# Kernel optimization log

Measured on AMD Instinct MI355X. Metric: run time of the kernel, lower is better.

Reference implementation:

```python
import jax, jax.numpy as jnp
import numpy as np

MASK_FILL = -987654321.0


def rotate_every_two(x):
    # pairs (x0, x1) -> (-x1, x0), interleaved back along last dim
    x1 = x[..., 0::2]
    x2 = x[..., 1::2]
    return jnp.stack((-x2, x1), axis=-1).reshape(x.shape)


def setup_inputs() -> dict:
    key = jax.random.key(0)
    ks = jax.random.split(key, 6)
    b, n, dim = 64, 197, 768
    heads, dim_head = 12, 64
    inner = heads * dim_head
    x = jax.random.normal(ks[0], (b, n, dim), dtype=jnp.float32)
    pos_emb = jax.random.normal(ks[1], (1, n, dim_head), dtype=jnp.float32)
    w_qkv = jax.random.normal(ks[2], (dim, 3 * inner), dtype=jnp.float32) * (dim ** -0.5)
    scale = jnp.full((heads,), dim_head ** -0.5, dtype=jnp.float32)
    w_out = jax.random.normal(ks[3], (inner, dim), dtype=jnp.float32) * (inner ** -0.5)
    b_out = jnp.zeros((dim,), dtype=jnp.float32)
    return {"x": x, "pos_emb": pos_emb, "w_qkv": w_qkv, "scale": scale,
            "w_out": w_out, "b_out": b_out}


def reference(x, pos_emb, w_qkv, scale, w_out, b_out):
    b, n, dim = x.shape
    h = scale.shape[0]
    qkv = x @ w_qkv                         # [b, n, 3*inner]
    q, k, v = jnp.split(qkv, 3, axis=-1)
    dh = q.shape[-1] // h
    to_heads = lambda t: t.reshape(b, n, h, dh).transpose(0, 2, 1, 3)  # bhnd
    q, k, v = to_heads(q), to_heads(k), to_heads(v)

    # RoPE: pos_emb [1, n, (2 * dh/2)] -> sin/cos [n, dh/2] -> interleave to [n, dh]
    sc = pos_emb[0].reshape(n, 2, dh // 2)
    sin = jnp.repeat(sc[:, 0], 2, axis=-1)  # [n, dh]
    cos = jnp.repeat(sc[:, 1], 2, axis=-1)
    q = q * cos + rotate_every_two(q) * sin
    k = k * cos + rotate_every_two(k) * sin

    # per-head learnable scale
    dots = jnp.einsum('bhid,bhjd->bhij', q, k) * scale[None, :, None, None]
    # diagonal (LSA) mask
    eye = jnp.eye(n, dtype=bool)
    dots = jnp.where(eye, MASK_FILL, dots)

    attn = jax.nn.softmax(dots, axis=-1)
    out = jnp.einsum('bhij,bhjd->bhid', attn, v)
    out = out.transpose(0, 2, 1, 3).reshape(b, n, h * dh)
    return out @ w_out + b_out
```

## Files before the change

kernel.cpp:

```cpp
#include <hip/hip_runtime.h>
#include <math.h>

#define MASK_FILL_F (-987654321.0f)

typedef unsigned short u16;
typedef unsigned int   u32;

constexpr int Bb   = 64;
constexpr int Ntok = 197;
constexpr int Dim  = 768;
constexpr int Heads= 12;
constexpr int Dh   = 64;
constexpr int Nq3  = 2304;
constexpr int Rows = 12608;
constexpr int Mpad = 12672;

using f32x4  = __attribute__((ext_vector_type(4))) float;
using bf16x8 = __attribute__((ext_vector_type(8))) short;

__device__ __forceinline__ u16 f2bf(float f) {
  u32 u = __float_as_uint(f);
  u = (u + 0x7fffu + ((u >> 16) & 1u)) >> 16;
  return (u16)u;
}

__device__ __forceinline__ void stage16(const void* gp, void* lp) {
  __builtin_amdgcn_global_load_lds(
      (const __attribute__((address_space(1))) u32*)gp,
      (__attribute__((address_space(3))) u32*)lp, 16, 0, 0);
}

__device__ __forceinline__ int sigma6(int M) {
  return (M & 0x23) | (((M >> 3) & 1) << 4) | (((M >> 2) & 1) << 3) |
         (((M >> 4) & 1) << 2);
}

__global__ __launch_bounds__(256) void cvt_bf16(const float* __restrict__ in,
                                                u16* __restrict__ out, int n4) {
  const int i = blockIdx.x * 256 + threadIdx.x;
  if (i < n4) {
    const float4 v = *(const float4*)&in[(size_t)i * 4];
    ushort4 u;
    u.x = f2bf(v.x); u.y = f2bf(v.y); u.z = f2bf(v.z); u.w = f2bf(v.w);
    *(ushort4*)&out[(size_t)i * 4] = u;
  }
}

__global__ __launch_bounds__(256) void transpose_cvt(const float* __restrict__ in,
                                                     u16* __restrict__ out,
                                                     int R, int C) {
  __shared__ float t[32][33];
  const int c0 = blockIdx.x * 32, r0 = blockIdx.y * 32;
  const int tx = threadIdx.x & 31, ty = threadIdx.x >> 5;
#pragma unroll
  for (int rr = ty; rr < 32; rr += 8)
    t[rr][tx] = in[(size_t)(r0 + rr) * C + c0 + tx];
  __syncthreads();
#pragma unroll
  for (int cc = ty; cc < 32; cc += 8)
    out[(size_t)(c0 + cc) * R + r0 + tx] = f2bf(t[tx][cc]);
}

__global__ __launch_bounds__(256) void vtrans(const u16* __restrict__ qkvB,
                                              u16* __restrict__ vT) {
  __shared__ u16 t[64 * 72];
  const int jt = blockIdx.x, bh = blockIdx.y;
  const int b = bh / Heads, h = bh % Heads;
  const int j0 = jt * 64;
  const int tid = threadIdx.x;

  for (int idx = tid; idx < 512; idx += 256) {
    const int jr = idx >> 3, c8 = (idx & 7) * 8;
    const int j = j0 + jr;
    uint4 u = make_uint4(0u, 0u, 0u, 0u);
    if (j < Ntok)
      u = *(const uint4*)(qkvB + (size_t)(b * Ntok + j) * Nq3 + 2 * Dim + h * Dh + c8);
    *(uint4*)&t[jr * 72 + c8] = u;
  }
  __syncthreads();
  for (int idx = tid; idx < 512; idx += 256) {
    const int d = idx >> 3, j8 = (idx & 7) * 8;
    ushort4 lo, hi;
    lo.x = t[(j8 + 0) * 72 + d]; lo.y = t[(j8 + 1) * 72 + d];
    lo.z = t[(j8 + 2) * 72 + d]; lo.w = t[(j8 + 3) * 72 + d];
    hi.x = t[(j8 + 4) * 72 + d]; hi.y = t[(j8 + 5) * 72 + d];
    hi.z = t[(j8 + 6) * 72 + d]; hi.w = t[(j8 + 7) * 72 + d];
    u16* dst = vT + ((size_t)bh * 64 + d) * 256 + j0 + j8;
    *(ushort4*)dst       = lo;
    *(ushort4*)(dst + 4) = hi;
  }
}

constexpr int Kc  = 768;
constexpr int NKT = Kc / 64;

#define BARM() asm volatile("s_barrier" ::: "memory")
#define VMW4() asm volatile("s_waitcnt vmcnt(4)" ::: "memory")

#define STGA(chunk, kt, BUF) \
  stage16(Ag + (size_t)(m0 + (chunk) * 8 + srow) * Kc + (kt) * 64 + scol, \
          &As[BUF][(chunk) * 512])
#define STGB(chunk, kt, BUF) \
  stage16(Bg + (size_t)(n0 + (chunk) * 8 + srow) * Kc + (kt) * 64 + scol, \
          &Bs[BUF][(chunk) * 512])

#define RDA(BUF, MH) \
  _Pragma("unroll") for (int m_ = 0; m_ < 4; ++m_) \
  _Pragma("unroll") for (int k_ = 0; k_ < 2; ++k_) \
    af[m_][k_] = *(const bf16x8*)&As[BUF][(wr * 128 + (MH) * 64 + m_ * 16 + tx) * 64 \
                                          + (((k_ * 4 + qd) ^ sx) * 8)];
#define RDB(BUF, NH, BFR) \
  _Pragma("unroll") for (int n_ = 0; n_ < 2; ++n_) \
  _Pragma("unroll") for (int k_ = 0; k_ < 2; ++k_) \
    BFR[n_][k_] = *(const bf16x8*)&Bs[BUF][(wc * 64 + (NH) * 32 + n_ * 16 + tx) * 64 \
                                           + (((k_ * 4 + qd) ^ sx) * 8)];

#define MM(MH, NH, BFR) \
  __builtin_amdgcn_s_setprio(1); \
  _Pragma("unroll") for (int m_ = 0; m_ < 4; ++m_) \
  _Pragma("unroll") for (int n_ = 0; n_ < 2; ++n_) \
  _Pragma("unroll") for (int k_ = 0; k_ < 2; ++k_) \
    acc[(MH) * 4 + m_][(NH) * 2 + n_] = __builtin_amdgcn_mfma_f32_16x16x32_bf16( \
        af[m_][k_], BFR[n_][k_], acc[(MH) * 4 + m_][(NH) * 2 + n_], 0, 0, 0); \
  __builtin_amdgcn_s_setprio(0);

template<int MODE, int TN>
__global__ __launch_bounds__(512, 2) void gemm8p(
    const u16* __restrict__ Ag, const u16* __restrict__ Bg,
    void* __restrict__ Cv, int Nn, int nwg,
    const float* __restrict__ pe, const float* __restrict__ bias)
{
  __shared__ u16 As[2][256 * 64];
  __shared__ u16 Bs[2][256 * 64];

  const int tid = threadIdx.x, lane = tid & 63, w = tid >> 6;

  const int orig = blockIdx.x;
  const int q8 = nwg >> 3, r8 = nwg & 7;
  const int xcd = orig & 7, sub = orig >> 3;
  const int wgid = (xcd < r8 ? xcd * (q8 + 1) : r8 * (q8 + 1) + (xcd - r8) * q8) + sub;
  const int tm = wgid / TN, tn = wgid % TN;
  const int m0 = tm * 256, n0 = tn * 256;

  const int wr = w >> 2, wc = w & 3;
  const int tx = lane & 15, qd = lane >> 4, sx = tx & 7;

  const int srow = lane >> 3;
  const int scol = ((lane & 7) ^ srow) * 8;
  const int b0 = (w >> 1) * 8 + (w & 1) * 2;

  STGA(w, 0, 0);        STGA(16 + w, 0, 0);
  STGB(b0 + 4, 0, 0);   STGB(b0 + 5, 0, 0);
  STGA(8 + w, 0, 0);    STGA(24 + w, 0, 0);
  STGB(b0, 0, 0);       STGB(b0 + 1, 0, 0);
  STGA(w, 1, 1);        STGA(16 + w, 1, 1);
  STGB(b0 + 4, 1, 1);   STGB(b0 + 5, 1, 1);
  VMW4();
  BARM();

  f32x4  acc[8][4] = {};
  bf16x8 af[4][2], bf0[2][2], bf1[2][2];

#pragma unroll 1
  for (int i = 0; i < NKT / 2; ++i) {
    const int u = 2 * i;
    RDA(0, 0); RDB(0, 0, bf0);
    STGA(8 + w, u + 1, 1); STGA(24 + w, u + 1, 1);
    BARM(); MM(0, 0, bf0); BARM();
    RDB(0, 1, bf1);
    STGB(b0, u + 1, 1); STGB(b0 + 1, u + 1, 1);
    BARM(); MM(0, 1, bf1); BARM();
    RDA(0, 1);
    STGA(w, u + 2, 0); STGA(16 + w, u + 2, 0);
    BARM(); MM(1, 1, bf1); BARM();
    STGB(b0 + 4, u + 2, 0); STGB(b0 + 5, u + 2, 0);
    BARM(); MM(1, 0, bf0); VMW4(); BARM();
    RDA(1, 0); RDB(1, 0, bf0);
    STGA(8 + w, u + 2, 0); STGA(24 + w, u + 2, 0);
    BARM(); MM(0, 0, bf0); BARM();
    RDB(1, 1, bf1);
    STGB(b0, u + 2, 0); STGB(b0 + 1, u + 2, 0);
    BARM(); MM(0, 1, bf1); BARM();
    RDA(1, 1);
    STGA(w, u + 3, 1); STGA(16 + w, u + 3, 1);
    BARM(); MM(1, 1, bf1); BARM();
    STGB(b0 + 4, u + 3, 1); STGB(b0 + 5, u + 3, 1);
    BARM(); MM(1, 0, bf0); VMW4(); BARM();
  }

  if (MODE == 0) {
    u16* C = (u16*)Cv;
    const bool dorot = (n0 < 2 * Dim);
#pragma unroll
    for (int mi = 0; mi < 8; ++mi) {
      const int rbase = m0 + wr * 128 + mi * 16 + qd * 4;
      int iq[4];
#pragma unroll
      for (int r = 0; r < 4; ++r) iq[r] = (rbase + r) % Ntok;
#pragma unroll
      for (int ni = 0; ni < 4; ++ni) {
        const int col = n0 + wc * 64 + ni * 16 + tx;
        const int mm  = (col & 63) >> 1;
        const int odd = col & 1;
#pragma unroll
        for (int r = 0; r < 4; ++r) {
          float v = acc[mi][ni][r];
          float res = v;
          if (dorot) {
            const float other = __shfl_xor(v, 1, 64);
            const float sn = pe[iq[r] * 64 + mm];
            const float c2 = pe[iq[r] * 64 + 32 + mm];
            res = odd ? (v * c2 + other * sn) : (v * c2 - other * sn);
          }
          C[(size_t)(rbase + r) * Nn + col] = f2bf(res);
        }
      }
    }
  } else {
    float* C = (float*)Cv;
#pragma unroll
    for (int mi = 0; mi < 8; ++mi) {
      const int rbase = m0 + wr * 128 + mi * 16 + qd * 4;
#pragma unroll
      for (int ni = 0; ni < 4; ++ni) {
        const int col = n0 + wc * 64 + ni * 16 + tx;
        const float bv = bias[col];
#pragma unroll
        for (int r = 0; r < 4; ++r) {
          const int row = rbase + r;
          if (row < Rows) C[(size_t)row * Nn + col] = acc[mi][ni][r] + bv;
        }
      }
    }
  }
}

constexpr int LS = 72;

__global__ __launch_bounds__(256) void attn7(
    const u16* __restrict__ qkvB, const u16* __restrict__ vT,
    const float* __restrict__ scale, u16* __restrict__ outB)
{
  __shared__ u16 ks [64 * LS];
  __shared__ u16 vts[64 * LS];

  const int it = blockIdx.x, bh = blockIdx.y;
  const int b = bh / Heads, h = bh % Heads;
  const int i0 = it * 128;
  const float sc = scale[h];
  const int tid = threadIdx.x, lane = tid & 63, w = tid >> 6;
  const int tx = lane & 15, q = lane >> 4;
  const size_t rowbase = (size_t)b * Ntok;

  bf16x8 bq[2][2];
#pragma unroll
  for (int g = 0; g < 2; ++g)
#pragma unroll
    for (int kk = 0; kk < 2; ++kk)
      bq[g][kk] = *(const bf16x8*)(qkvB +
          (rowbase + i0 + 32 * w + 16 * g + tx) * (size_t)Nq3 + h * Dh + kk * 32 + q * 8);

  float l_part[2] = {0.f, 0.f};
  f32x4 oacc[2][4] = {};

  for (int jt = 0; jt < 4; ++jt) {
    const int j0 = jt * 64;
    __syncthreads();

    for (int idx = tid; idx < 512; idx += 256) {
      const int M = idx >> 3, c8 = (idx & 7) * 8;
      const int js = sigma6(M);
      *(uint4*)&ks[M * LS + c8] =
          *(const uint4*)(qkvB + (rowbase + j0 + js) * (size_t)Nq3 + Dim + h * Dh + c8);
    }
    for (int idx = tid; idx < 512; idx += 256) {
      const int d = idx >> 3, c8 = (idx & 7) * 8;
      *(uint4*)&vts[d * LS + c8] =
          *(const uint4*)(vT + ((size_t)bh * 64 + d) * 256 + j0 + c8);
    }
    __syncthreads();

#pragma unroll
    for (int g = 0; g < 2; ++g) {
      f32x4 sT[4] = {};
#pragma unroll
      for (int kk = 0; kk < 2; ++kk)
#pragma unroll
        for (int jb = 0; jb < 4; ++jb) {
          const bf16x8 ka = *(const bf16x8*)&ks[(jb * 16 + tx) * LS + kk * 32 + q * 8];
          sT[jb] = __builtin_amdgcn_mfma_f32_16x16x32_bf16(ka, bq[g][kk], sT[jb], 0, 0, 0);
        }

      const int ig = i0 + 32 * w + 16 * g + tx;
      union { bf16x8 v; u16 e[8]; } pk[2];
      float lp = 0.f;
#pragma unroll
      for (int jb = 0; jb < 4; ++jb)
#pragma unroll
        for (int r = 0; r < 4; ++r) {
          const int jg = j0 + 32 * (jb >> 1) + 8 * q + 4 * (jb & 1) + r;
          const float s = fminf(sT[jb][r] * sc, 80.f);
          const bool bad = (jg >= Ntok) || (jg == ig);
          const float p = bad ? 0.f : __expf(s);
          lp += p;
          pk[jb >> 1].e[(jb & 1) * 4 + r] = f2bf(p);
        }
      l_part[g] += lp;

#pragma unroll
      for (int kk = 0; kk < 2; ++kk)
#pragma unroll
        for (int nb = 0; nb < 4; ++nb) {
          const bf16x8 vb = *(const bf16x8*)&vts[(nb * 16 + tx) * LS + kk * 32 + q * 8];
          oacc[g][nb] = __builtin_amdgcn_mfma_f32_16x16x32_bf16(pk[kk].v, vb,
                                                               oacc[g][nb], 0, 0, 0);
        }
    }
  }

#pragma unroll
  for (int g = 0; g < 2; ++g) {
    float l = l_part[g];
    l += __shfl_xor(l, 16, 64);
    l += __shfl_xor(l, 32, 64);
    const float linv = 1.0f / l;
#pragma unroll
    for (int r = 0; r < 4; ++r) {
      const float lr = __shfl(linv, 4 * q + r, 64);
      const int igr = i0 + 32 * w + 16 * g + 4 * q + r;
      if (igr < Ntok) {
#pragma unroll
        for (int nb = 0; nb < 4; ++nb)
          outB[(rowbase + igr) * (size_t)Dim + h * Dh + nb * 16 + tx] =
              f2bf(oacc[g][nb][r] * lr);
      }
    }
  }
}

extern "C" void kernel_launch(void* const* d_in, const int* in_sizes, int n_in,
                              void* d_out, int out_size, void* d_ws, size_t ws_size,
                              hipStream_t stream) {
  const float* x     = (const float*)d_in[0];
  const float* pe    = (const float*)d_in[1];
  const float* w_qkv = (const float*)d_in[2];
  const float* scale = (const float*)d_in[3];
  const float* w_out = (const float*)d_in[4];
  const float* b_out = (const float*)d_in[5];
  float* out = (float*)d_out;

  u16* xb    = (u16*)d_ws;
  u16* wqkvT = xb    + (size_t)Mpad * Dim;
  u16* woutT = wqkvT + (size_t)Nq3 * Dim;
  u16* qkvB  = woutT + (size_t)Dim * Dim;
  u16* attnB = qkvB  + (size_t)Mpad * Nq3;
  u16* vT    = attnB + (size_t)Mpad * Dim;

  cvt_bf16<<<(Rows * Dim / 4 + 255) / 256, 256, 0, stream>>>(x, xb, Rows * Dim / 4);
  transpose_cvt<<<dim3(Nq3 / 32, Dim / 32), 256, 0, stream>>>(w_qkv, wqkvT, Dim, Nq3);
  transpose_cvt<<<dim3(Dim / 32, Dim / 32), 256, 0, stream>>>(w_out, woutT, Dim, Dim);

  constexpr int NWG0 = 50 * 9;
  gemm8p<0, 9><<<NWG0, 512, 0, stream>>>(xb, wqkvT, qkvB, Nq3, NWG0, pe, nullptr);

  vtrans<<<dim3(4, Bb * Heads), 256, 0, stream>>>(qkvB, vT);

  attn7<<<dim3(2, Bb * Heads), 256, 0, stream>>>(qkvB, vT, scale, attnB);

  constexpr int NWG1 = 50 * 3;
  gemm8p<1, 3><<<NWG1, 512, 0, stream>>>(attnB, woutT, out, Dim, NWG1, nullptr, b_out);
}
```

Before: 282.9 us.

## Fuse V transpose into QKV GEMM epilogue and use smaller-tile output GEMM

The QKV GEMM epilogue now handles V-column tiles itself. It stages them through shared memory and writes V transposed straight into the vT buffer, so the separate vtrans kernel is removed. The output projection moves from the 256x256 pipelined GEMM to a simpler 128x128 tile GEMM, giving more workgroups for the 768-wide output. The K-tile prefetch index is clamped so the pipeline no longer reads past the end. The transposed V writes are scattered 2-byte stores, and the attention kernel now zeroes padded tokens in V explicitly.

```diff
diff --git a/kernel.cpp b/kernel.cpp
--- a/kernel.cpp
+++ b/kernel.cpp
@@ -61,58 +61,30 @@
     out[(size_t)(c0 + cc) * R + r0 + tx] = f2bf(t[tx][cc]);
 }
 
-__global__ __launch_bounds__(256) void vtrans(const u16* __restrict__ qkvB,
-                                              u16* __restrict__ vT) {
-  __shared__ u16 t[64 * 72];
-  const int jt = blockIdx.x, bh = blockIdx.y;
-  const int b = bh / Heads, h = bh % Heads;
-  const int j0 = jt * 64;
-  const int tid = threadIdx.x;
-
-  for (int idx = tid; idx < 512; idx += 256) {
-    const int jr = idx >> 3, c8 = (idx & 7) * 8;
-    const int j = j0 + jr;
-    uint4 u = make_uint4(0u, 0u, 0u, 0u);
-    if (j < Ntok)
-      u = *(const uint4*)(qkvB + (size_t)(b * Ntok + j) * Nq3 + 2 * Dim + h * Dh + c8);
-    *(uint4*)&t[jr * 72 + c8] = u;
-  }
-  __syncthreads();
-  for (int idx = tid; idx < 512; idx += 256) {
-    const int d = idx >> 3, j8 = (idx & 7) * 8;
-    ushort4 lo, hi;
-    lo.x = t[(j8 + 0) * 72 + d]; lo.y = t[(j8 + 1) * 72 + d];
-    lo.z = t[(j8 + 2) * 72 + d]; lo.w = t[(j8 + 3) * 72 + d];
-    hi.x = t[(j8 + 4) * 72 + d]; hi.y = t[(j8 + 5) * 72 + d];
-    hi.z = t[(j8 + 6) * 72 + d]; hi.w = t[(j8 + 7) * 72 + d];
-    u16* dst = vT + ((size_t)bh * 64 + d) * 256 + j0 + j8;
-    *(ushort4*)dst       = lo;
-    *(ushort4*)(dst + 4) = hi;
-  }
-}
-
 constexpr int Kc  = 768;
 constexpr int NKT = Kc / 64;
+#define KTC(x) ((x) < NKT ? (x) : (NKT - 1))
 
 #define BARM() asm volatile("s_barrier" ::: "memory")
 #define VMW4() asm volatile("s_waitcnt vmcnt(4)" ::: "memory")
+#define VMW0() asm volatile("s_waitcnt vmcnt(0)" ::: "memory")
 
 #define STGA(chunk, kt, BUF) \
   stage16(Ag + (size_t)(m0 + (chunk) * 8 + srow) * Kc + (kt) * 64 + scol, \
-          &As[BUF][(chunk) * 512])
+          &SH[BUF][(chunk) * 512])
 #define STGB(chunk, kt, BUF) \
   stage16(Bg + (size_t)(n0 + (chunk) * 8 + srow) * Kc + (kt) * 64 + scol, \
-          &Bs[BUF][(chunk) * 512])
+          &SH[2 + (BUF)][(chunk) * 512])
 
 #define RDA(BUF, MH) \
   _Pragma("unroll") for (int m_ = 0; m_ < 4; ++m_) \
   _Pragma("unroll") for (int k_ = 0; k_ < 2; ++k_) \
-    af[m_][k_] = *(const bf16x8*)&As[BUF][(wr * 128 + (MH) * 64 + m_ * 16 + tx) * 64 \
+    af[m_][k_] = *(const bf16x8*)&SH[BUF][(wr * 128 + (MH) * 64 + m_ * 16 + tx) * 64 \
                                           + (((k_ * 4 + qd) ^ sx) * 8)];
 #define RDB(BUF, NH, BFR) \
   _Pragma("unroll") for (int n_ = 0; n_ < 2; ++n_) \
   _Pragma("unroll") for (int k_ = 0; k_ < 2; ++k_) \
-    BFR[n_][k_] = *(const bf16x8*)&Bs[BUF][(wc * 64 + (NH) * 32 + n_ * 16 + tx) * 64 \
+    BFR[n_][k_] = *(const bf16x8*)&SH[2 + (BUF)][(wc * 64 + (NH) * 32 + n_ * 16 + tx) * 64 \
                                            + (((k_ * 4 + qd) ^ sx) * 8)];
 
 #define MM(MH, NH, BFR) \
@@ -124,14 +96,13 @@
         af[m_][k_], BFR[n_][k_], acc[(MH) * 4 + m_][(NH) * 2 + n_], 0, 0, 0); \
   __builtin_amdgcn_s_setprio(0);
 
-template<int MODE, int TN>
+template<int TN>
 __global__ __launch_bounds__(512, 2) void gemm8p(
     const u16* __restrict__ Ag, const u16* __restrict__ Bg,
-    void* __restrict__ Cv, int Nn, int nwg,
-    const float* __restrict__ pe, const float* __restrict__ bias)
+    u16* __restrict__ Cb, u16* __restrict__ vT, int Nn, int nwg,
+    const float* __restrict__ pe)
 {
-  __shared__ u16 As[2][256 * 64];
-  __shared__ u16 Bs[2][256 * 64];
+  __shared__ u16 SH[4][256 * 64];
 
   const int tid = threadIdx.x, lane = tid & 63, w = tid >> 6;
 
@@ -171,26 +142,24 @@
     STGB(b0, u + 1, 1); STGB(b0 + 1, u + 1, 1);
     BARM(); MM(0, 1, bf1); BARM();
     RDA(0, 1);
-    STGA(w, u + 2, 0); STGA(16 + w, u + 2, 0);
+    STGA(w, KTC(u + 2), 0); STGA(16 + w, KTC(u + 2), 0);
     BARM(); MM(1, 1, bf1); BARM();
-    STGB(b0 + 4, u + 2, 0); STGB(b0 + 5, u + 2, 0);
+    STGB(b0 + 4, KTC(u + 2), 0); STGB(b0 + 5, KTC(u + 2), 0);
     BARM(); MM(1, 0, bf0); VMW4(); BARM();
     RDA(1, 0); RDB(1, 0, bf0);
-    STGA(8 + w, u + 2, 0); STGA(24 + w, u + 2, 0);
+    STGA(8 + w, KTC(u + 2), 0); STGA(24 + w, KTC(u + 2), 0);
     BARM(); MM(0, 0, bf0); BARM();
     RDB(1, 1, bf1);
-    STGB(b0, u + 2, 0); STGB(b0 + 1, u + 2, 0);
+    STGB(b0, KTC(u + 2), 0); STGB(b0 + 1, KTC(u + 2), 0);
     BARM(); MM(0, 1, bf1); BARM();
     RDA(1, 1);
-    STGA(w, u + 3, 1); STGA(16 + w, u + 3, 1);
+    STGA(w, KTC(u + 3), 1); STGA(16 + w, KTC(u + 3), 1);
     BARM(); MM(1, 1, bf1); BARM();
-    STGB(b0 + 4, u + 3, 1); STGB(b0 + 5, u + 3, 1);
+    STGB(b0 + 4, KTC(u + 3), 1); STGB(b0 + 5, KTC(u + 3), 1);
     BARM(); MM(1, 0, bf0); VMW4(); BARM();
   }
 
-  if (MODE == 0) {
-    u16* C = (u16*)Cv;
-    const bool dorot = (n0 < 2 * Dim);
+  if (n0 < 2 * Dim) {
 #pragma unroll
     for (int mi = 0; mi < 8; ++mi) {
       const int rbase = m0 + wr * 128 + mi * 16 + qd * 4;
@@ -205,31 +174,103 @@
 #pragma unroll
         for (int r = 0; r < 4; ++r) {
           float v = acc[mi][ni][r];
-          float res = v;
-          if (dorot) {
-            const float other = __shfl_xor(v, 1, 64);
-            const float sn = pe[iq[r] * 64 + mm];
-            const float c2 = pe[iq[r] * 64 + 32 + mm];
-            res = odd ? (v * c2 + other * sn) : (v * c2 - other * sn);
-          }
-          C[(size_t)(rbase + r) * Nn + col] = f2bf(res);
+          const float other = __shfl_xor(v, 1, 64);
+          const float sn = pe[iq[r] * 64 + mm];
+          const float c2 = pe[iq[r] * 64 + 32 + mm];
+          const float res = odd ? (v * c2 + other * sn) : (v * c2 - other * sn);
+          Cb[(size_t)(rbase + r) * Nn + col] = f2bf(res);
         }
       }
     }
   } else {
-    float* C = (float*)Cv;
+    VMW0();
+    BARM();
+    u16* T = &SH[0][0];
 #pragma unroll
     for (int mi = 0; mi < 8; ++mi) {
-      const int rbase = m0 + wr * 128 + mi * 16 + qd * 4;
+      const int rowIn = wr * 128 + mi * 16 + qd * 4;
 #pragma unroll
       for (int ni = 0; ni < 4; ++ni) {
-        const int col = n0 + wc * 64 + ni * 16 + tx;
-        const float bv = bias[col];
-#pragma unroll
-        for (int r = 0; r < 4; ++r) {
-          const int row = rbase + r;
-          if (row < Rows) C[(size_t)row * Nn + col] = acc[mi][ni][r] + bv;
+        const int nIn = wc * 64 + ni * 16 + tx;
+        const u32 base = (u32)nIn * 512 + (((u32)rowIn * 2) ^ ((u32)(nIn & 7) << 4));
+        const u32 p01 = (u32)f2bf(acc[mi][ni][0]) | ((u32)f2bf(acc[mi][ni][1]) << 16);
+        const u32 p23 = (u32)f2bf(acc[mi][ni][2]) | ((u32)f2bf(acc[mi][ni][3]) << 16);
+        *(u32*)((char*)T + base)     = p01;
+        *(u32*)((char*)T + base + 4) = p23;
+      }
+    }
+    __syncthreads();
+    const int hbase = (n0 - 2 * Dim) >> 6;
+    const int nI = tid >> 1, half = tid & 1;
+    const int dd = nI & 63, hh = hbase + (nI >> 6);
+    u16* vrow = vT + ((size_t)0 * 64) ;
+    (void)vrow;
+#pragma unroll
+    for (int k = 0; k < 16; ++k) {
+      const int rowIn0 = (half * 16 + k) * 8;
+      const u32 a = (u32)nI * 512 + (((u32)rowIn0 * 2) ^ ((u32)(nI & 7) << 4));
+      const bf16x8 vv = *(const bf16x8*)((char*)T + a);
+#pragma unroll
+      for (int e = 0; e < 8; ++e) {
+        const int gr = m0 + rowIn0 + e;
+        if (gr < Rows) {
+          const int bB = gr / 197;
+          const int jj = gr - bB * 197;
+          vT[((size_t)(bB * Heads + hh) * 64 + dd) * 256 + jj] = (u16)vv[e];
         }
+      }
+    }
+  }
+}
+
+__global__ __launch_bounds__(256) void gemm_bt1(
+    const u16* __restrict__ Ag, const u16* __restrict__ Bg,
+    float* __restrict__ C, int K, int Nn, const float* __restrict__ bias)
+{
+  __shared__ u16 As[128 * 32];
+  __shared__ u16 Bs[128 * 32];
+  const int tid = threadIdx.x, lane = tid & 63, w = tid >> 6;
+  const int m0 = blockIdx.y * 128, n0 = blockIdx.x * 128;
+  const int wm = (w & 1) * 64, wn = (w >> 1) * 64;
+  const int tx = lane & 15, qk = lane >> 4;
+  const int rs = lane >> 2, cs = (lane & 3) * 8;
+
+  f32x4 acc[4][4] = {};
+
+  for (int k0 = 0; k0 < K; k0 += 32) {
+#pragma unroll
+    for (int t = 0; t < 2; ++t) {
+      const int r0 = w * 16 + t * 64;
+      stage16(Ag + (size_t)(m0 + r0 + rs) * K + k0 + cs, &As[r0 * 32]);
+      stage16(Bg + (size_t)(n0 + r0 + rs) * K + k0 + cs, &Bs[r0 * 32]);
+    }
+    __syncthreads();
+    bf16x8 af[4], bf[4];
+#pragma unroll
+    for (int f = 0; f < 4; ++f) {
+      af[f] = *(const bf16x8*)&As[(wm + f * 16 + tx) * 32 + qk * 8];
+      bf[f] = *(const bf16x8*)&Bs[(wn + f * 16 + tx) * 32 + qk * 8];
+    }
+#pragma unroll
+    for (int fm = 0; fm < 4; ++fm)
+#pragma unroll
+      for (int fn = 0; fn < 4; ++fn)
+        acc[fm][fn] = __builtin_amdgcn_mfma_f32_16x16x32_bf16(
+            af[fm], bf[fn], acc[fm][fn], 0, 0, 0);
+    __syncthreads();
+  }
+
+#pragma unroll
+  for (int fm = 0; fm < 4; ++fm) {
+    const int rbase = m0 + wm + fm * 16 + qk * 4;
+#pragma unroll
+    for (int fn = 0; fn < 4; ++fn) {
+      const int col = n0 + wn + fn * 16 + tx;
+      const float bv = bias[col];
+#pragma unroll
+      for (int r = 0; r < 4; ++r) {
+        const int row = rbase + r;
+        if (row < Rows) C[(size_t)row * Nn + col] = acc[fm][fn][r] + bv;
       }
     }
   }
@@ -275,8 +316,14 @@
     }
     for (int idx = tid; idx < 512; idx += 256) {
       const int d = idx >> 3, c8 = (idx & 7) * 8;
-      *(uint4*)&vts[d * LS + c8] =
-          *(const uint4*)(vT + ((size_t)bh * 64 + d) * 256 + j0 + c8);
+      uint4 u = *(const uint4*)(vT + ((size_t)bh * 64 + d) * 256 + j0 + c8);
+      if (j0 + c8 + 8 > Ntok) {
+        u16* e = (u16*)&u;
+#pragma unroll
+        for (int t2 = 0; t2 < 8; ++t2)
+          if (j0 + c8 + t2 >= Ntok) e[t2] = 0;
+      }
+      *(uint4*)&vts[d * LS + c8] = u;
     }
     __syncthreads();
 
@@ -361,12 +408,10 @@
   transpose_cvt<<<dim3(Dim / 32, Dim / 32), 256, 0, stream>>>(w_out, woutT, Dim, Dim);
 
   constexpr int NWG0 = 50 * 9;
-  gemm8p<0, 9><<<NWG0, 512, 0, stream>>>(xb, wqkvT, qkvB, Nq3, NWG0, pe, nullptr);
-
-  vtrans<<<dim3(4, Bb * Heads), 256, 0, stream>>>(qkvB, vT);
+  gemm8p<9><<<NWG0, 512, 0, stream>>>(xb, wqkvT, qkvB, vT, Nq3, NWG0, pe);
 
   attn7<<<dim3(2, Bb * Heads), 256, 0, stream>>>(qkvB, vT, scale, attnB);
 
-  constexpr int NWG1 = 50 * 3;
-  gemm8p<1, 3><<<NWG1, 512, 0, stream>>>(attnB, woutT, out, Dim, NWG1, nullptr, b_out);
-}
+  gemm_bt1<<<dim3(Dim / 128, Mpad / 128), 256, 0, stream>>>(
+      attnB, woutT, out, Dim, Dim, b_out);
+}
```

New measurement: 284.8 us. No clear change (+0.7%).
